# Kernel tuning notes

Measured on AMD Instinct MI355X. Metric: run time of the kernel, lower is better.

## Reference

```python
import jax, jax.numpy as jnp
import numpy as np
import math

H = 1024  # hidden_dim
NH = 16   # num_heads
HD = H // NH  # head_dim = 64
B, S, C = 2, 2048, 256  # batch, seq_len, cond_len
EPS = 1e-5


def layernorm(x, g, b):
    m = jnp.mean(x, axis=-1, keepdims=True)
    v = jnp.var(x, axis=-1, keepdims=True)
    return (x - m) * jax.lax.rsqrt(v + EPS) * g + b


def apply_rope(x, freqs):
    # x: [b, s, h, d], freqs broadcastable to [b, s, h, d//2]
    cos, sin = jnp.cos(freqs), jnp.sin(freqs)
    x1, x2 = jnp.split(x, 2, axis=-1)
    return jnp.concatenate([x1 * cos - x2 * sin, x2 * cos + x1 * sin], axis=-1)


def setup_inputs() -> dict:
    key = jax.random.key(0)
    ks = jax.random.split(key, 16)
    sc = 0.02
    x = jax.random.normal(ks[0], (B, S, H), jnp.float32)
    # rope freqs: positions * inv_freq over half head dim
    inv_freq = 1.0 / (10000.0 ** (jnp.arange(HD // 2, dtype=jnp.float32) / (HD // 2)))
    rope_freqs = (jnp.arange(S, dtype=jnp.float32)[:, None] * inv_freq[None, :]).reshape(S, 1, HD // 2)
    # causal additive mask [1,1,S,S]
    causal = jnp.tril(jnp.ones((S, S), dtype=bool))
    attention_mask = jnp.where(causal, 0.0, -1e9).astype(jnp.float32)[None, None]
    conditioning = jax.random.normal(ks[1], (B, C, H), jnp.float32)
    conditioning_mask = jnp.zeros((B, 1, 1, C), jnp.float32)
    params = dict(
        ln1_g=jnp.ones((H,)), ln1_b=jnp.zeros((H,)),
        ln2_g=jnp.ones((H,)), ln2_b=jnp.zeros((H,)),
        lnc_g=jnp.ones((H,)), lnc_b=jnp.zeros((H,)),
        w_qkv=jax.random.normal(ks[2], (H, 3 * H)) * sc,
        w_out=jax.random.normal(ks[3], (H, H)) * sc, b_out=jnp.zeros((H,)),
        w_cq=jax.random.normal(ks[4], (H, H)) * sc,
        w_ckv=jax.random.normal(ks[5], (H, 2 * H)) * sc,
        w_cout=jax.random.normal(ks[6], (H, H)) * sc, b_cout=jnp.zeros((H,)),
        w_ff1=jax.random.normal(ks[7], (H, 4 * H)) * sc, b_ff1=jnp.zeros((4 * H,)),
        w_ff2=jax.random.normal(ks[8], (4 * H, H)) * sc, b_ff2=jnp.zeros((H,)),
    )
    return dict(x=x, rope_freqs=rope_freqs, attention_mask=attention_mask,
                conditioning=conditioning, conditioning_mask=conditioning_mask, **params)


def reference(x, rope_freqs, attention_mask, conditioning, conditioning_mask,
              ln1_g, ln1_b, ln2_g, ln2_b, lnc_g, lnc_b,
              w_qkv, w_out, b_out, w_cq, w_ckv, w_cout, b_cout,
              w_ff1, b_ff1, w_ff2, b_ff2):
    scale = 1.0 / math.sqrt(HD)
    # --- causal self-attention ---
    residual = x
    h = layernorm(x, ln1_g, ln1_b)
    qkv = h @ w_qkv  # [b,s,3H]
    q, k, v = jnp.split(qkv, 3, axis=-1)
    q = q.reshape(B, S, NH, HD)
    k = k.reshape(B, S, NH, HD)
    v = v.reshape(B, S, NH, HD)
    q = apply_rope(q, rope_freqs)
    k = apply_rope(k, rope_freqs)
    scores = jnp.einsum('bqhd,bkhd->bhqk', q, k) * scale + attention_mask
    attn = jax.nn.softmax(scores, axis=-1)
    out = jnp.einsum('bhqk,bkhd->bqhd', attn, v).reshape(B, S, H)
    x = residual + out @ w_out + b_out
    # --- cross-attention ---
    residual = x
    h = layernorm(x, lnc_g, lnc_b)
    q = (h @ w_cq).reshape(B, S, NH, HD)
    kv = conditioning @ w_ckv
    k, v = jnp.split(kv, 2, axis=-1)
    k = k.reshape(B, C, NH, HD)
    v = v.reshape(B, C, NH, HD)
    scores = jnp.einsum('bqhd,bkhd->bhqk', q, k) * scale + conditioning_mask
    attn = jax.nn.softmax(scores, axis=-1)
    out = jnp.einsum('bhqk,bkhd->bqhd', attn, v).reshape(B, S, H)
    x = residual + out @ w_cout + b_cout
    # --- FFN ---
    residual = x
    h = layernorm(x, ln2_g, ln2_b)
    h = jax.nn.gelu(h @ w_ff1 + b_ff1, approximate=False)
    x = residual + h @ w_ff2 + b_ff2
    return x
```

## Files before the change

### kernel.cpp

```cpp
#include <hip/hip_runtime.h>

#define HDIM   1024
#define NHEADS 16
#define HEADD  64
#define BATCH  2
#define SEQ    2048
#define CLEN   256
#define NROWS  (BATCH*SEQ)
#define SCALE  0.125f

typedef __bf16 bf16x8 __attribute__((ext_vector_type(8)));
typedef float  f32x4  __attribute__((ext_vector_type(4)));

__device__ __forceinline__ unsigned short f2bf(float f) {
  union { float f; unsigned int u; } x; x.f = f;
  unsigned int r = x.u + 0x7fffu + ((x.u >> 16) & 1u);
  return (unsigned short)(r >> 16);
}
__device__ __forceinline__ float bf2f(unsigned short u) {
  union { unsigned int u; float f; } x; x.u = ((unsigned int)u) << 16;
  return x.f;
}

__device__ __forceinline__ void gl2lds16(const unsigned short* g, unsigned short* l) {
  __builtin_amdgcn_global_load_lds(
      (const __attribute__((address_space(1))) unsigned int*)g,
      (__attribute__((address_space(3))) unsigned int*)l, 16, 0, 0);
}

__global__ __launch_bounds__(256)
void cast_transpose64(const float* __restrict__ in, unsigned short* __restrict__ out,
                      int K, int N) {
  __shared__ float t[64][68];
  const int kb = blockIdx.y * 64, nb = blockIdx.x * 64;
  const int tid = threadIdx.x;
  const int r = tid >> 4, c = (tid & 15) * 4;
#pragma unroll
  for (int i = 0; i < 4; ++i) {
    float4 v = *(const float4*)(in + (size_t)(kb + r + i * 16) * N + nb + c);
    t[r + i * 16][c]     = v.x;
    t[r + i * 16][c + 1] = v.y;
    t[r + i * 16][c + 2] = v.z;
    t[r + i * 16][c + 3] = v.w;
  }
  __syncthreads();
  const int nr = tid >> 3, kc = (tid & 7) * 8;
#pragma unroll
  for (int i = 0; i < 2; ++i) {
    unsigned short us[8];
#pragma unroll
    for (int j = 0; j < 8; ++j) us[j] = f2bf(t[kc + j][nr + i * 32]);
    *(uint4*)(out + (size_t)(nb + nr + i * 32) * K + kb + kc) = *(uint4*)us;
  }
}

__global__ void cast_kernel8(const float* __restrict__ in, unsigned short* __restrict__ out, int n8) {
  int i = blockIdx.x * 256 + threadIdx.x;
  if (i < n8) {
    float4 a = ((const float4*)in)[2 * i], b = ((const float4*)in)[2 * i + 1];
    unsigned short us[8] = { f2bf(a.x), f2bf(a.y), f2bf(a.z), f2bf(a.w),
                             f2bf(b.x), f2bf(b.y), f2bf(b.z), f2bf(b.w) };
    ((uint4*)out)[i] = *(uint4*)us;
  }
}

__global__ __launch_bounds__(256)
void vtrans_kernel(const unsigned short* __restrict__ in, int str, int voff, int rows,
                   unsigned short* __restrict__ out) {
  __shared__ unsigned short t[64][72];
  const int h = blockIdx.y & (NHEADS - 1), b = blockIdx.y >> 4;
  const int s0 = blockIdx.x * 64;
  const int tid = threadIdx.x;
  const int r = tid >> 2, c = (tid & 3) * 16;
  const unsigned short* src = in + (size_t)(b * rows + s0 + r) * str + voff + h * 64 + c;
  *(uint4*)(&t[r][c])     = *(const uint4*)(src);
  *(uint4*)(&t[r][c + 8]) = *(const uint4*)(src + 8);
  __syncthreads();
  const int d = tid >> 2, sc = (tid & 3) * 16;
  unsigned short tmp[16];
#pragma unroll
  for (int i = 0; i < 16; ++i) tmp[i] = t[sc + i][d];
  unsigned short* dst = out + ((size_t)(b * NHEADS + h) * 64 + d) * rows + s0 + sc;
  *(uint4*)(dst)     = *(uint4*)(tmp);
  *(uint4*)(dst + 8) = *(uint4*)(tmp + 8);
}

__global__ __launch_bounds__(256)
void layernorm_kernel(const float* __restrict__ x, const float* __restrict__ g,
                      const float* __restrict__ b, unsigned short* __restrict__ out) {
  int row = blockIdx.x;
  const float4 v = ((const float4*)(x + (size_t)row * HDIM))[threadIdx.x];
  float s  = v.x + v.y + v.z + v.w;
  float sq = v.x*v.x + v.y*v.y + v.z*v.z + v.w*v.w;
  for (int o = 32; o; o >>= 1) { s += __shfl_xor(s, o); sq += __shfl_xor(sq, o); }
  __shared__ float rs[4], rq[4];
  int wave = threadIdx.x >> 6;
  if ((threadIdx.x & 63) == 0) { rs[wave] = s; rq[wave] = sq; }
  __syncthreads();
  s  = rs[0] + rs[1] + rs[2] + rs[3];
  sq = rq[0] + rq[1] + rq[2] + rq[3];
  float mean = s * (1.f/HDIM);
  float var  = sq * (1.f/HDIM) - mean*mean;
  float rstd = rsqrtf(var + 1e-5f);
  float4 gg = ((const float4*)g)[threadIdx.x];
  float4 bb = ((const float4*)b)[threadIdx.x];
  ushort4 o;
  o.x = f2bf((v.x - mean) * rstd * gg.x + bb.x);
  o.y = f2bf((v.y - mean) * rstd * gg.y + bb.y);
  o.z = f2bf((v.z - mean) * rstd * gg.z + bb.z);
  o.w = f2bf((v.w - mean) * rstd * gg.w + bb.w);
  ((ushort4*)(out + (size_t)row * HDIM))[threadIdx.x] = o;
}

template<int TBM, int TBN, bool BIAS, bool RES, bool GELU_, bool OUTBF>
__global__ __launch_bounds__(256)
void gemm_bt(const unsigned short* __restrict__ A, const unsigned short* __restrict__ Bt,
             const float* __restrict__ bias, const float* __restrict__ res,
             void* __restrict__ out, int M, int N, int K) {
  constexpr int MR = TBM / 32;
  constexpr int NR = TBN / 32;
  __shared__ unsigned short Al[2][TBM * 64];
  __shared__ unsigned short Bl[2][TBN * 64];
  const int tid  = threadIdx.x;
  const int wave = tid >> 6, lane = tid & 63;
  const int wr = wave >> 1, wc = wave & 1;
  const int nwg = gridDim.x * gridDim.y;
  int lin = blockIdx.y * gridDim.x + blockIdx.x;
  lin = (lin & 7) * (nwg >> 3) + (lin >> 3);
  const int m0 = (lin / gridDim.x) * TBM, n0 = (lin % gridDim.x) * TBN;
  const int lrow = lane & 15, hi = lane >> 4;
  const int rx = lrow & 7;

  f32x4 acc[MR][NR] = {};

  const int trow = tid >> 3, pslot = tid & 7;
  const int lcol = (pslot ^ (trow & 7)) * 8;
  const unsigned short* ga = A  + (size_t)(m0 + trow) * K + lcol;
  const unsigned short* gb = Bt + (size_t)(n0 + trow) * K + lcol;
  const int ldst = trow * 64 + pslot * 8;
  const int nt = K >> 6;

#pragma unroll
  for (int i = 0; i < MR; ++i)
    gl2lds16(ga + (size_t)i * 32 * K, Al[0] + ldst + i * 32 * 64);
#pragma unroll
  for (int i = 0; i < NR; ++i)
    gl2lds16(gb + (size_t)i * 32 * K, Bl[0] + ldst + i * 32 * 64);
  __syncthreads();

  int cur = 0;
  for (int t = 0; t < nt; ++t) {
    if (t + 1 < nt) {
      const int k1 = (t + 1) << 6;
#pragma unroll
      for (int i = 0; i < MR; ++i)
        gl2lds16(ga + (size_t)i * 32 * K + k1, Al[cur ^ 1] + ldst + i * 32 * 64);
#pragma unroll
      for (int i = 0; i < NR; ++i)
        gl2lds16(gb + (size_t)i * 32 * K + k1, Bl[cur ^ 1] + ldst + i * 32 * 64);
    }
#pragma unroll
    for (int kk = 0; kk < 2; ++kk) {
      const int cslot = ((kk << 2) | hi);
      const int coff  = (cslot ^ rx) * 8;
      bf16x8 af[MR], bfr[NR];
#pragma unroll
      for (int m = 0; m < MR; ++m)
        af[m] = *(const bf16x8*)(Al[cur] + (wr*(TBM/2) + m*16 + lrow) * 64 + coff);
#pragma unroll
      for (int n = 0; n < NR; ++n)
        bfr[n] = *(const bf16x8*)(Bl[cur] + (wc*(TBN/2) + n*16 + lrow) * 64 + coff);
#pragma unroll
      for (int m = 0; m < MR; ++m)
#pragma unroll
        for (int n = 0; n < NR; ++n)
          acc[m][n] = __builtin_amdgcn_mfma_f32_16x16x32_bf16(af[m], bfr[n], acc[m][n], 0, 0, 0);
    }
    __syncthreads();
    cur ^= 1;
  }

#pragma unroll
  for (int m = 0; m < MR; ++m)
#pragma unroll
    for (int n = 0; n < NR; ++n)
#pragma unroll
      for (int r = 0; r < 4; ++r) {
        int row = m0 + wr*(TBM/2) + m*16 + hi * 4 + r;
        int col = n0 + wc*(TBN/2) + n*16 + lrow;
        float v = acc[m][n][r];
        if (BIAS)  v += bias[col];
        if (GELU_) v = 0.5f * v * (1.0f + erff(v * 0.70710678118654752f));
        if (RES)   v += res[(size_t)row * N + col];
        if (OUTBF) ((unsigned short*)out)[(size_t)row * N + col] = f2bf(v);
        else       ((float*)out)[(size_t)row * N + col] = v;
      }
}

__global__ void rope_kernel(unsigned short* __restrict__ qkv, const float* __restrict__ freqs) {
  int idx = blockIdx.x * 256 + threadIdx.x;
  int d = idx & 31;
  int h = (idx >> 5) & 15;
  int row = idx >> 9;
  int s = row & (SEQ - 1);
  float f = freqs[s * 32 + d];
  float sn, cs;
  sincosf(f, &sn, &cs);
  size_t base = (size_t)row * 3072 + h * 64 + d;
  float x1 = bf2f(qkv[base]), x2 = bf2f(qkv[base + 32]);
  qkv[base]      = f2bf(x1 * cs - x2 * sn);
  qkv[base + 32] = f2bf(x2 * cs + x1 * sn);
  float y1 = bf2f(qkv[base + 1024]), y2 = bf2f(qkv[base + 1024 + 32]);
  qkv[base + 1024]      = f2bf(y1 * cs - y2 * sn);
  qkv[base + 1024 + 32] = f2bf(y2 * cs + y1 * sn);
}

#define QT 64
#define KT 64

__global__ __launch_bounds__(512)
void flash_attn_causal8(const unsigned short* __restrict__ qp, int qstr,
                        const unsigned short* __restrict__ kp, int kstr,
                        const unsigned short* __restrict__ vt,
                        unsigned short* __restrict__ outp) {
  __shared__ unsigned short Kl[2][KT][72];
  __shared__ unsigned short Vt[2][64][72];
  __shared__ unsigned short Pl[8][16][72];

  const int h = blockIdx.y & (NHEADS - 1), b = blockIdx.y >> 4;
  const int tid = threadIdx.x;
  const int wave = tid >> 6, lane = tid & 63;
  const int grp = wave >> 2, w4 = wave & 3;
  const int lo = lane & 15, hi = lane >> 4;
  const int NQB = SEQ / QT;
  float* mb = (float*)&Pl[0][0][0];

  const unsigned short* vbase = vt + (size_t)(b * NHEADS + h) * 64 * SEQ;

  for (int pass = 0; pass < 2; ++pass) {
    const int qblk = pass == 0 ? (int)blockIdx.x : NQB - 1 - (int)blockIdx.x;
    const int q0 = qblk * QT;
    const int qw = q0 + w4 * 16;

    bf16x8 qf[2];
    {
      const unsigned short* qb = qp + (size_t)(b * SEQ + qw + lo) * qstr + h * 64 + hi * 8;
      qf[0] = *(const bf16x8*)(qb);
      qf[1] = *(const bf16x8*)(qb + 32);
    }

    f32x4 o_acc[4] = {};
    float mrow[4], lrow[4];
#pragma unroll
    for (int r = 0; r < 4; ++r) { mrow[r] = -1e30f; lrow[r] = 0.f; }

    const int T = qblk + 1;
    const int iters = (T + 1) >> 1;
    for (int it = 0; it < iters; ++it) {
      const int t = 2 * it + grp;
      const bool act = t < T;
      const int j0 = t * KT;
      __syncthreads();
      if (act) {
        int tg = tid & 255;
        int r = tg >> 2, c = (tg & 3) * 16;
        const unsigned short* ksrc = kp + (size_t)(b * SEQ + j0 + r) * kstr + h * 64 + c;
        *(uint4*)(&Kl[grp][r][c])     = *(const uint4*)(ksrc);
        *(uint4*)(&Kl[grp][r][c + 8]) = *(const uint4*)(ksrc + 8);
        const unsigned short* vsrc = vbase + (size_t)r * SEQ + j0 + c;
        *(uint4*)(&Vt[grp][r][c])     = *(const uint4*)(vsrc);
        *(uint4*)(&Vt[grp][r][c + 8]) = *(const uint4*)(vsrc + 8);
      }
      __syncthreads();
      if (act) {
        f32x4 s[4] = {};
#pragma unroll
        for (int n = 0; n < 4; ++n) {
          bf16x8 b0 = *(const bf16x8*)(&Kl[grp][n * 16 + lo][hi * 8]);
          bf16x8 b1 = *(const bf16x8*)(&Kl[grp][n * 16 + lo][32 + hi * 8]);
          s[n] = __builtin_amdgcn_mfma_f32_16x16x32_bf16(qf[0], b0, s[n], 0, 0, 0);
          s[n] = __builtin_amdgcn_mfma_f32_16x16x32_bf16(qf[1], b1, s[n], 0, 0, 0);
        }
        if (t == T - 1) {
#pragma unroll
          for (int n = 0; n < 4; ++n)
#pragma unroll
            for (int r = 0; r < 4; ++r)
              if (j0 + n * 16 + lo > qw + hi * 4 + r) s[n][r] = -1e30f;
        }
        float pr[4][4];
#pragma unroll
        for (int r = 0; r < 4; ++r) {
          float mx = -1e30f;
#pragma unroll
          for (int n = 0; n < 4; ++n) {
            float v = s[n][r] * SCALE;
            s[n][r] = v;
            mx = fmaxf(mx, v);
          }
          mx = fmaxf(mx, __shfl_xor(mx, 1));
          mx = fmaxf(mx, __shfl_xor(mx, 2));
          mx = fmaxf(mx, __shfl_xor(mx, 4));
          mx = fmaxf(mx, __shfl_xor(mx, 8));
          const float mnew = fmaxf(mrow[r], mx);
          const float corr = __expf(mrow[r] - mnew);
          mrow[r] = mnew;
          float ls = 0.f;
#pragma unroll
          for (int n = 0; n < 4; ++n) {
            float p = __expf(s[n][r] - mnew);
            pr[n][r] = p;
            ls += p;
          }
          ls += __shfl_xor(ls, 1);
          ls += __shfl_xor(ls, 2);
          ls += __shfl_xor(ls, 4);
          ls += __shfl_xor(ls, 8);
          lrow[r] = lrow[r] * corr + ls;
#pragma unroll
          for (int n2 = 0; n2 < 4; ++n2) o_acc[n2][r] *= corr;
        }
#pragma unroll
        for (int n = 0; n < 4; ++n)
#pragma unroll
          for (int r = 0; r < 4; ++r)
            Pl[wave][hi * 4 + r][n * 16 + lo] = f2bf(pr[n][r]);

        bf16x8 pa0 = *(const bf16x8*)(&Pl[wave][lo][hi * 8]);
        bf16x8 pa1 = *(const bf16x8*)(&Pl[wave][lo][32 + hi * 8]);
#pragma unroll
        for (int n = 0; n < 4; ++n) {
          bf16x8 vb0 = *(const bf16x8*)(&Vt[grp][n * 16 + lo][hi * 8]);
          bf16x8 vb1 = *(const bf16x8*)(&Vt[grp][n * 16 + lo][32 + hi * 8]);
          o_acc[n] = __builtin_amdgcn_mfma_f32_16x16x32_bf16(pa0, vb0, o_acc[n], 0, 0, 0);
          o_acc[n] = __builtin_amdgcn_mfma_f32_16x16x32_bf16(pa1, vb1, o_acc[n], 0, 0, 0);
        }
      }
    }

    unsigned short* ob = outp + (size_t)(b * SEQ + qw) * HDIM + h * 64;
#pragma unroll
    for (int half = 0; half < 2; ++half) {
      __syncthreads();
      if (grp == 1) {
        float* dst = mb + (w4 * 64 + lane) * 13;
#pragma unroll
        for (int rr = 0; rr < 2; ++rr) {
          int r = half * 2 + rr;
          dst[rr * 6]     = mrow[r];
          dst[rr * 6 + 1] = lrow[r];
#pragma unroll
          for (int n = 0; n < 4; ++n) dst[rr * 6 + 2 + n] = o_acc[n][r];
        }
      }
      __syncthreads();
      if (grp == 0) {
        const float* s1 = mb + (w4 * 64 + lane) * 13;
#pragma unroll
        for (int rr = 0; rr < 2; ++rr) {
          int r = half * 2 + rr;
          float m1 = s1[rr * 6], l1 = s1[rr * 6 + 1];
          float M  = fmaxf(mrow[r], m1);
          float c0 = __expf(mrow[r] - M), c1 = __expf(m1 - M);
          float inv = 1.f / (lrow[r] * c0 + l1 * c1);
#pragma unroll
          for (int n = 0; n < 4; ++n) {
            float o = o_acc[n][r] * c0 + s1[rr * 6 + 2 + n] * c1;
            ob[(size_t)(hi * 4 + r) * HDIM + n * 16 + lo] = f2bf(o * inv);
          }
        }
      }
    }
    __syncthreads();
  }
}

__global__ __launch_bounds__(256)
void flash_attn_cross(const unsigned short* __restrict__ qp, int qstr,
                      const unsigned short* __restrict__ kp, int kstr,
                      const unsigned short* __restrict__ vt,
                      int kvrows, const float* __restrict__ mask,
                      unsigned short* __restrict__ outp) {
  __shared__ unsigned short Kl[KT][72];
  __shared__ unsigned short Vt[64][72];
  __shared__ unsigned short Pl[4][16][72];

  const int h = blockIdx.y & (NHEADS - 1), b = blockIdx.y >> 4;
  const int wave = threadIdx.x >> 6, lane = threadIdx.x & 63;
  const int lo = lane & 15, hi = lane >> 4;
  const int q0 = blockIdx.x * QT;
  const int qw = q0 + wave * 16;

  const unsigned short* vbase = vt + (size_t)(b * NHEADS + h) * 64 * kvrows;

  bf16x8 qf[2];
  {
    const unsigned short* qb = qp + (size_t)(b * SEQ + qw + lo) * qstr + h * 64 + hi * 8;
    qf[0] = *(const bf16x8*)(qb);
    qf[1] = *(const bf16x8*)(qb + 32);
  }

  f32x4 o_acc[4] = {};
  float mrow[4], lrow[4];
#pragma unroll
  for (int r = 0; r < 4; ++r) { mrow[r] = -1e30f; lrow[r] = 0.f; }

  const int ntiles = kvrows / KT;
  for (int t = 0; t < ntiles; ++t) {
    const int j0 = t * KT;
    __syncthreads();
    {
      int r = threadIdx.x >> 2, c = (threadIdx.x & 3) * 16;
      const unsigned short* ksrc = kp + (size_t)(b * kvrows + j0 + r) * kstr + h * 64 + c;
      *(uint4*)(&Kl[r][c])     = *(const uint4*)(ksrc);
      *(uint4*)(&Kl[r][c + 8]) = *(const uint4*)(ksrc + 8);
      const unsigned short* vsrc = vbase + (size_t)r * kvrows + j0 + c;
      *(uint4*)(&Vt[r][c])     = *(const uint4*)(vsrc);
      *(uint4*)(&Vt[r][c + 8]) = *(const uint4*)(vsrc + 8);
    }
    __syncthreads();

    f32x4 s[4] = {};
#pragma unroll
    for (int n = 0; n < 4; ++n) {
      bf16x8 b0 = *(const bf16x8*)(&Kl[n * 16 + lo][hi * 8]);
      bf16x8 b1 = *(const bf16x8*)(&Kl[n * 16 + lo][32 + hi * 8]);
      s[n] = __builtin_amdgcn_mfma_f32_16x16x32_bf16(qf[0], b0, s[n], 0, 0, 0);
      s[n] = __builtin_amdgcn_mfma_f32_16x16x32_bf16(qf[1], b1, s[n], 0, 0, 0);
    }

    float mk[4];
#pragma unroll
    for (int n = 0; n < 4; ++n) mk[n] = mask[b * kvrows + j0 + n * 16 + lo];

    float pr[4][4];
#pragma unroll
    for (int r = 0; r < 4; ++r) {
      float mx = -1e30f;
#pragma unroll
      for (int n = 0; n < 4; ++n) {
        float v = s[n][r] * SCALE + mk[n];
        s[n][r] = v;
        mx = fmaxf(mx, v);
      }
      mx = fmaxf(mx, __shfl_xor(mx, 1));
      mx = fmaxf(mx, __shfl_xor(mx, 2));
      mx = fmaxf(mx, __shfl_xor(mx, 4));
      mx = fmaxf(mx, __shfl_xor(mx, 8));
      const float mnew = fmaxf(mrow[r], mx);
      const float corr = __expf(mrow[r] - mnew);
      mrow[r] = mnew;
      float ls = 0.f;
#pragma unroll
      for (int n = 0; n < 4; ++n) {
        float p = __expf(s[n][r] - mnew);
        pr[n][r] = p;
        ls += p;
      }
      ls += __shfl_xor(ls, 1);
      ls += __shfl_xor(ls, 2);
      ls += __shfl_xor(ls, 4);
      ls += __shfl_xor(ls, 8);
      lrow[r] = lrow[r] * corr + ls;
#pragma unroll
      for (int n2 = 0; n2 < 4; ++n2) o_acc[n2][r] *= corr;
    }

#pragma unroll
    for (int n = 0; n < 4; ++n)
#pragma unroll
      for (int r = 0; r < 4; ++r)
        Pl[wave][hi * 4 + r][n * 16 + lo] = f2bf(pr[n][r]);

    bf16x8 pa0 = *(const bf16x8*)(&Pl[wave][lo][hi * 8]);
    bf16x8 pa1 = *(const bf16x8*)(&Pl[wave][lo][32 + hi * 8]);
#pragma unroll
    for (int n = 0; n < 4; ++n) {
      bf16x8 vb0 = *(const bf16x8*)(&Vt[n * 16 + lo][hi * 8]);
      bf16x8 vb1 = *(const bf16x8*)(&Vt[n * 16 + lo][32 + hi * 8]);
      o_acc[n] = __builtin_amdgcn_mfma_f32_16x16x32_bf16(pa0, vb0, o_acc[n], 0, 0, 0);
      o_acc[n] = __builtin_amdgcn_mfma_f32_16x16x32_bf16(pa1, vb1, o_acc[n], 0, 0, 0);
    }
  }

  unsigned short* ob = outp + (size_t)(b * SEQ + qw) * HDIM + h * 64;
#pragma unroll
  for (int r = 0; r < 4; ++r) {
    const float inv = 1.f / lrow[r];
#pragma unroll
    for (int n = 0; n < 4; ++n)
      ob[(size_t)(hi * 4 + r) * HDIM + n * 16 + lo] = f2bf(o_acc[n][r] * inv);
  }
}

extern "C" void kernel_launch(void* const* d_in, const int* in_sizes, int n_in,
                              void* d_out, int out_size, void* d_ws, size_t ws_size,
                              hipStream_t stream) {
  const float* x      = (const float*)d_in[0];
  const float* rfreq  = (const float*)d_in[1];
  const float* cond   = (const float*)d_in[3];
  const float* cmask  = (const float*)d_in[4];
  const float* ln1_g  = (const float*)d_in[5];
  const float* ln1_b  = (const float*)d_in[6];
  const float* ln2_g  = (const float*)d_in[7];
  const float* ln2_b  = (const float*)d_in[8];
  const float* lnc_g  = (const float*)d_in[9];
  const float* lnc_b  = (const float*)d_in[10];
  const float* w_qkv  = (const float*)d_in[11];
  const float* w_out  = (const float*)d_in[12];
  const float* b_out  = (const float*)d_in[13];
  const float* w_cq   = (const float*)d_in[14];
  const float* w_ckv  = (const float*)d_in[15];
  const float* w_cout = (const float*)d_in[16];
  const float* b_cout = (const float*)d_in[17];
  const float* w_ff1  = (const float*)d_in[18];
  const float* b_ff1  = (const float*)d_in[19];
  const float* w_ff2  = (const float*)d_in[20];
  const float* b_ff2  = (const float*)d_in[21];

  char* ws = (char*)d_ws;
  size_t off = 0;
  auto alloc = [&](size_t bytes) { size_t r = off; off += (bytes + 255) & ~(size_t)255; return r; };
  unsigned short* wt_qkv  = (unsigned short*)(ws + alloc((size_t)3072*1024*2));
  unsigned short* wt_out  = (unsigned short*)(ws + alloc((size_t)1024*1024*2));
  unsigned short* wt_cq   = (unsigned short*)(ws + alloc((size_t)1024*1024*2));
  unsigned short* wt_ckv  = (unsigned short*)(ws + alloc((size_t)2048*1024*2));
  unsigned short* wt_cout = (unsigned short*)(ws + alloc((size_t)1024*1024*2));
  unsigned short* wt_ff1  = (unsigned short*)(ws + alloc((size_t)4096*1024*2));
  unsigned short* wt_ff2  = (unsigned short*)(ws + alloc((size_t)1024*4096*2));
  unsigned short* condb   = (unsigned short*)(ws + alloc((size_t)512*1024*2));
  unsigned short* hbuf    = (unsigned short*)(ws + alloc((size_t)NROWS*1024*2));
  unsigned short* big     = (unsigned short*)(ws + alloc((size_t)NROWS*4096*2));
  unsigned short* attnb   = (unsigned short*)(ws + alloc((size_t)NROWS*1024*2));
  float*          x1      = (float*)(ws + alloc((size_t)NROWS*1024*4));
  unsigned short* kvc     = (unsigned short*)(ws + alloc((size_t)512*2048*2));
  unsigned short* vts     = (unsigned short*)(ws + alloc((size_t)BATCH*NHEADS*64*SEQ*2));
  unsigned short* vtc     = (unsigned short*)(ws + alloc((size_t)BATCH*NHEADS*64*CLEN*2));
  float*          outf    = (float*)d_out;

  cast_transpose64<<<dim3(48, 16), 256, 0, stream>>>(w_qkv,  wt_qkv,  1024, 3072);
  cast_transpose64<<<dim3(16, 16), 256, 0, stream>>>(w_out,  wt_out,  1024, 1024);
  cast_transpose64<<<dim3(16, 16), 256, 0, stream>>>(w_cq,   wt_cq,   1024, 1024);
  cast_transpose64<<<dim3(32, 16), 256, 0, stream>>>(w_ckv,  wt_ckv,  1024, 2048);
  cast_transpose64<<<dim3(16, 16), 256, 0, stream>>>(w_cout, wt_cout, 1024, 1024);
  cast_transpose64<<<dim3(64, 16), 256, 0, stream>>>(w_ff1,  wt_ff1,  1024, 4096);
  cast_transpose64<<<dim3(16, 64), 256, 0, stream>>>(w_ff2,  wt_ff2,  4096, 1024);
  cast_kernel8<<<(512*1024/8 + 255)/256, 256, 0, stream>>>(cond, condb, 512*1024/8);

  layernorm_kernel<<<NROWS, 256, 0, stream>>>(x, ln1_g, ln1_b, hbuf);
  gemm_bt<128,128,false,false,false,true><<<dim3(3072/128, NROWS/128), 256, 0, stream>>>(
      hbuf, wt_qkv, nullptr, nullptr, big, NROWS, 3072, 1024);
  rope_kernel<<<(NROWS*NHEADS*32)/256, 256, 0, stream>>>(big, rfreq);
  vtrans_kernel<<<dim3(SEQ/64, BATCH*NHEADS), 256, 0, stream>>>(big, 3072, 2048, SEQ, vts);
  flash_attn_causal8<<<dim3(SEQ/QT/2, BATCH*NHEADS), 512, 0, stream>>>(
      big, 3072, big + 1024, 3072, vts, attnb);
  gemm_bt<128,64,true,true,false,false><<<dim3(1024/64, NROWS/128), 256, 0, stream>>>(
      attnb, wt_out, b_out, x, x1, NROWS, 1024, 1024);

  layernorm_kernel<<<NROWS, 256, 0, stream>>>(x1, lnc_g, lnc_b, hbuf);
  gemm_bt<128,64,false,false,false,true><<<dim3(1024/64, NROWS/128), 256, 0, stream>>>(
      hbuf, wt_cq, nullptr, nullptr, big, NROWS, 1024, 1024);
  gemm_bt<64,64,false,false,false,true><<<dim3(2048/64, 512/64), 256, 0, stream>>>(
      condb, wt_ckv, nullptr, nullptr, kvc, 512, 2048, 1024);
  vtrans_kernel<<<dim3(CLEN/64, BATCH*NHEADS), 256, 0, stream>>>(kvc, 2048, 1024, CLEN, vtc);
  flash_attn_cross<<<dim3(SEQ/QT, BATCH*NHEADS), 256, 0, stream>>>(
      big, 1024, kvc, 2048, vtc, CLEN, cmask, attnb);
  gemm_bt<128,64,true,true,false,false><<<dim3(1024/64, NROWS/128), 256, 0, stream>>>(
      attnb, wt_cout, b_cout, x1, outf, NROWS, 1024, 1024);

  layernorm_kernel<<<NROWS, 256, 0, stream>>>(outf, ln2_g, ln2_b, hbuf);
  gemm_bt<128,128,true,false,true,true><<<dim3(4096/128, NROWS/128), 256, 0, stream>>>(
      hbuf, wt_ff1, b_ff1, nullptr, big, NROWS, 4096, 1024);
  gemm_bt<128,64,true,true,false,false><<<dim3(1024/64, NROWS/128), 256, 0, stream>>>(
      big, wt_ff2, b_ff2, outf, outf, NROWS, 1024, 4096);
}
```

Baseline: 370.3 us.

## Double-buffer flash attention K/V tiles via async global-to-LDS loads with swizzle

Replaces the 512-thread causal attention kernel, which split KV tiles across two wave groups and merged their partial results, with a 256-thread kernel. It double-buffers K/V tiles using direct global-to-LDS loads, prefetching the next tile while the current one is computed. LDS tiles now use an XOR-swizzled unpadded layout to avoid bank conflicts, and softmax uses exp2 with the log2e factor folded into the scale. The cross-attention kernel gets the same treatment. The trade-off is less intra-block parallelism per query block and one barrier per tile, in exchange for overlapped loads and no cross-group merge.

```diff
diff --git a/kernel.cpp b/kernel.cpp
--- a/kernel.cpp
+++ b/kernel.cpp
@@ -8,6 +8,7 @@
 #define CLEN   256
 #define NROWS  (BATCH*SEQ)
 #define SCALE  0.125f
+#define LOG2E  1.44269504088896f
 
 typedef __bf16 bf16x8 __attribute__((ext_vector_type(8)));
 typedef float  f32x4  __attribute__((ext_vector_type(4)));
@@ -215,32 +216,33 @@
   qkv[base + 1024 + 32] = f2bf(y2 * cs + y1 * sn);
 }
 
-#define QT 64
-#define KT 64
-
-__global__ __launch_bounds__(512)
-void flash_attn_causal8(const unsigned short* __restrict__ qp, int qstr,
+__global__ __launch_bounds__(256)
+void flash_attn_causal4(const unsigned short* __restrict__ qp, int qstr,
                         const unsigned short* __restrict__ kp, int kstr,
                         const unsigned short* __restrict__ vt,
                         unsigned short* __restrict__ outp) {
-  __shared__ unsigned short Kl[2][KT][72];
-  __shared__ unsigned short Vt[2][64][72];
-  __shared__ unsigned short Pl[8][16][72];
+  __shared__ unsigned short Kl[2][64 * 64];
+  __shared__ unsigned short Vl[2][64 * 64];
+  __shared__ unsigned short Pl[4][16][72];
 
   const int h = blockIdx.y & (NHEADS - 1), b = blockIdx.y >> 4;
   const int tid = threadIdx.x;
   const int wave = tid >> 6, lane = tid & 63;
-  const int grp = wave >> 2, w4 = wave & 3;
   const int lo = lane & 15, hi = lane >> 4;
-  const int NQB = SEQ / QT;
-  float* mb = (float*)&Pl[0][0][0];
+  const int NQB = SEQ / 64;
+  const float SC2 = SCALE * LOG2E;
 
   const unsigned short* vbase = vt + (size_t)(b * NHEADS + h) * 64 * SEQ;
+  const int trow = tid >> 3, pslot = tid & 7;
+  const int lcol = (pslot ^ (trow & 7)) * 8;
+  const int ldst = tid * 8;
+  const int x7 = lo & 7;
+  const int c0 = (hi ^ x7) * 8, c1 = ((hi + 4) ^ x7) * 8;
 
   for (int pass = 0; pass < 2; ++pass) {
     const int qblk = pass == 0 ? (int)blockIdx.x : NQB - 1 - (int)blockIdx.x;
-    const int q0 = qblk * QT;
-    const int qw = q0 + w4 * 16;
+    const int q0 = qblk * 64;
+    const int qw = q0 + wave * 16;
 
     bf16x8 qf[2];
     {
@@ -255,123 +257,105 @@
     for (int r = 0; r < 4; ++r) { mrow[r] = -1e30f; lrow[r] = 0.f; }
 
     const int T = qblk + 1;
-    const int iters = (T + 1) >> 1;
-    for (int it = 0; it < iters; ++it) {
-      const int t = 2 * it + grp;
-      const bool act = t < T;
-      const int j0 = t * KT;
+    {
+      const unsigned short* ks = kp + (size_t)(b * SEQ + trow) * kstr + h * 64 + lcol;
+      const unsigned short* vs = vbase + (size_t)trow * SEQ + lcol;
+      gl2lds16(ks, Kl[0] + ldst);
+      gl2lds16(ks + (size_t)32 * kstr, Kl[0] + ldst + 32 * 64);
+      gl2lds16(vs, Vl[0] + ldst);
+      gl2lds16(vs + (size_t)32 * SEQ, Vl[0] + ldst + 32 * 64);
+    }
+    __syncthreads();
+
+    int cur = 0;
+    for (int t = 0; t < T; ++t) {
+      if (t + 1 < T) {
+        const int j1 = (t + 1) * 64;
+        const unsigned short* ks = kp + (size_t)(b * SEQ + j1 + trow) * kstr + h * 64 + lcol;
+        const unsigned short* vs = vbase + (size_t)trow * SEQ + j1 + lcol;
+        gl2lds16(ks, Kl[cur ^ 1] + ldst);
+        gl2lds16(ks + (size_t)32 * kstr, Kl[cur ^ 1] + ldst + 32 * 64);
+        gl2lds16(vs, Vl[cur ^ 1] + ldst);
+        gl2lds16(vs + (size_t)32 * SEQ, Vl[cur ^ 1] + ldst + 32 * 64);
+      }
+      const unsigned short* Kc = Kl[cur];
+      const unsigned short* Vc = Vl[cur];
+      const int j0 = t * 64;
+
+      f32x4 s[4] = {};
+#pragma unroll
+      for (int n = 0; n < 4; ++n) {
+        bf16x8 b0 = *(const bf16x8*)(Kc + (n * 16 + lo) * 64 + c0);
+        bf16x8 b1 = *(const bf16x8*)(Kc + (n * 16 + lo) * 64 + c1);
+        s[n] = __builtin_amdgcn_mfma_f32_16x16x32_bf16(qf[0], b0, s[n], 0, 0, 0);
+        s[n] = __builtin_amdgcn_mfma_f32_16x16x32_bf16(qf[1], b1, s[n], 0, 0, 0);
+      }
+      if (t == T - 1) {
+#pragma unroll
+        for (int n = 0; n < 4; ++n)
+#pragma unroll
+          for (int r = 0; r < 4; ++r)
+            if (j0 + n * 16 + lo > qw + hi * 4 + r) s[n][r] = -1e30f;
+      }
+      float pr[4][4];
+#pragma unroll
+      for (int r = 0; r < 4; ++r) {
+        float mx = -1e30f;
+#pragma unroll
+        for (int n = 0; n < 4; ++n) {
+          float v = s[n][r] * SC2;
+          s[n][r] = v;
+          mx = fmaxf(mx, v);
+        }
+        mx = fmaxf(mx, __shfl_xor(mx, 1));
+        mx = fmaxf(mx, __shfl_xor(mx, 2));
+        mx = fmaxf(mx, __shfl_xor(mx, 4));
+        mx = fmaxf(mx, __shfl_xor(mx, 8));
+        const float mnew = fmaxf(mrow[r], mx);
+        const float corr = exp2f(mrow[r] - mnew);
+        mrow[r] = mnew;
+        float ls = 0.f;
+#pragma unroll
+        for (int n = 0; n < 4; ++n) {
+          float p = exp2f(s[n][r] - mnew);
+          pr[n][r] = p;
+          ls += p;
+        }
+        ls += __shfl_xor(ls, 1);
+        ls += __shfl_xor(ls, 2);
+        ls += __shfl_xor(ls, 4);
+        ls += __shfl_xor(ls, 8);
+        lrow[r] = lrow[r] * corr + ls;
+#pragma unroll
+        for (int n2 = 0; n2 < 4; ++n2) o_acc[n2][r] *= corr;
+      }
+#pragma unroll
+      for (int n = 0; n < 4; ++n)
+#pragma unroll
+        for (int r = 0; r < 4; ++r)
+          Pl[wave][hi * 4 + r][n * 16 + lo] = f2bf(pr[n][r]);
+
+      bf16x8 pa0 = *(const bf16x8*)(&Pl[wave][lo][hi * 8]);
+      bf16x8 pa1 = *(const bf16x8*)(&Pl[wave][lo][32 + hi * 8]);
+#pragma unroll
+      for (int n = 0; n < 4; ++n) {
+        bf16x8 vb0 = *(const bf16x8*)(Vc + (n * 16 + lo) * 64 + c0);
+        bf16x8 vb1 = *(const bf16x8*)(Vc + (n * 16 + lo) * 64 + c1);
+        o_acc[n] = __builtin_amdgcn_mfma_f32_16x16x32_bf16(pa0, vb0, o_acc[n], 0, 0, 0);
+        o_acc[n] = __builtin_amdgcn_mfma_f32_16x16x32_bf16(pa1, vb1, o_acc[n], 0, 0, 0);
+      }
       __syncthreads();
-      if (act) {
-        int tg = tid & 255;
-        int r = tg >> 2, c = (tg & 3) * 16;
-        const unsigned short* ksrc = kp + (size_t)(b * SEQ + j0 + r) * kstr + h * 64 + c;
-        *(uint4*)(&Kl[grp][r][c])     = *(const uint4*)(ksrc);
-        *(uint4*)(&Kl[grp][r][c + 8]) = *(const uint4*)(ksrc + 8);
-        const unsigned short* vsrc = vbase + (size_t)r * SEQ + j0 + c;
-        *(uint4*)(&Vt[grp][r][c])     = *(const uint4*)(vsrc);
-        *(uint4*)(&Vt[grp][r][c + 8]) = *(const uint4*)(vsrc + 8);
-      }
-      __syncthreads();
-      if (act) {
-        f32x4 s[4] = {};
-#pragma unroll
-        for (int n = 0; n < 4; ++n) {
-          bf16x8 b0 = *(const bf16x8*)(&Kl[grp][n * 16 + lo][hi * 8]);
-          bf16x8 b1 = *(const bf16x8*)(&Kl[grp][n * 16 + lo][32 + hi * 8]);
-          s[n] = __builtin_amdgcn_mfma_f32_16x16x32_bf16(qf[0], b0, s[n], 0, 0, 0);
-          s[n] = __builtin_amdgcn_mfma_f32_16x16x32_bf16(qf[1], b1, s[n], 0, 0, 0);
-        }
-        if (t == T - 1) {
-#pragma unroll
-          for (int n = 0; n < 4; ++n)
-#pragma unroll
-            for (int r = 0; r < 4; ++r)
-              if (j0 + n * 16 + lo > qw + hi * 4 + r) s[n][r] = -1e30f;
-        }
-        float pr[4][4];
-#pragma unroll
-        for (int r = 0; r < 4; ++r) {
-          float mx = -1e30f;
-#pragma unroll
-          for (int n = 0; n < 4; ++n) {
-            float v = s[n][r] * SCALE;
-            s[n][r] = v;
-            mx = fmaxf(mx, v);
-          }
-          mx = fmaxf(mx, __shfl_xor(mx, 1));
-          mx = fmaxf(mx, __shfl_xor(mx, 2));
-          mx = fmaxf(mx, __shfl_xor(mx, 4));
-          mx = fmaxf(mx, __shfl_xor(mx, 8));
-          const float mnew = fmaxf(mrow[r], mx);
-          const float corr = __expf(mrow[r] - mnew);
-          mrow[r] = mnew;
-          float ls = 0.f;
-#pragma unroll
-          for (int n = 0; n < 4; ++n) {
-            float p = __expf(s[n][r] - mnew);
-            pr[n][r] = p;
-            ls += p;
-          }
-          ls += __shfl_xor(ls, 1);
-          ls += __shfl_xor(ls, 2);
-          ls += __shfl_xor(ls, 4);
-          ls += __shfl_xor(ls, 8);
-          lrow[r] = lrow[r] * corr + ls;
-#pragma unroll
-          for (int n2 = 0; n2 < 4; ++n2) o_acc[n2][r] *= corr;
-        }
-#pragma unroll
-        for (int n = 0; n < 4; ++n)
-#pragma unroll
-          for (int r = 0; r < 4; ++r)
-            Pl[wave][hi * 4 + r][n * 16 + lo] = f2bf(pr[n][r]);
-
-        bf16x8 pa0 = *(const bf16x8*)(&Pl[wave][lo][hi * 8]);
-        bf16x8 pa1 = *(const bf16x8*)(&Pl[wave][lo][32 + hi * 8]);
-#pragma unroll
-        for (int n = 0; n < 4; ++n) {
-          bf16x8 vb0 = *(const bf16x8*)(&Vt[grp][n * 16 + lo][hi * 8]);
-          bf16x8 vb1 = *(const bf16x8*)(&Vt[grp][n * 16 + lo][32 + hi * 8]);
-          o_acc[n] = __builtin_amdgcn_mfma_f32_16x16x32_bf16(pa0, vb0, o_acc[n], 0, 0, 0);
-          o_acc[n] = __builtin_amdgcn_mfma_f32_16x16x32_bf16(pa1, vb1, o_acc[n], 0, 0, 0);
-        }
-      }
+      cur ^= 1;
     }
 
     unsigned short* ob = outp + (size_t)(b * SEQ + qw) * HDIM + h * 64;
 #pragma unroll
-    for (int half = 0; half < 2; ++half) {
-      __syncthreads();
-      if (grp == 1) {
-        float* dst = mb + (w4 * 64 + lane) * 13;
-#pragma unroll
-        for (int rr = 0; rr < 2; ++rr) {
-          int r = half * 2 + rr;
-          dst[rr * 6]     = mrow[r];
-          dst[rr * 6 + 1] = lrow[r];
-#pragma unroll
-          for (int n = 0; n < 4; ++n) dst[rr * 6 + 2 + n] = o_acc[n][r];
-        }
-      }
-      __syncthreads();
-      if (grp == 0) {
-        const float* s1 = mb + (w4 * 64 + lane) * 13;
-#pragma unroll
-        for (int rr = 0; rr < 2; ++rr) {
-          int r = half * 2 + rr;
-          float m1 = s1[rr * 6], l1 = s1[rr * 6 + 1];
-          float M  = fmaxf(mrow[r], m1);
-          float c0 = __expf(mrow[r] - M), c1 = __expf(m1 - M);
-          float inv = 1.f / (lrow[r] * c0 + l1 * c1);
-#pragma unroll
-          for (int n = 0; n < 4; ++n) {
-            float o = o_acc[n][r] * c0 + s1[rr * 6 + 2 + n] * c1;
-            ob[(size_t)(hi * 4 + r) * HDIM + n * 16 + lo] = f2bf(o * inv);
-          }
-        }
-      }
-    }
-    __syncthreads();
+    for (int r = 0; r < 4; ++r) {
+      const float inv = 1.f / lrow[r];
+#pragma unroll
+      for (int n = 0; n < 4; ++n)
+        ob[(size_t)(hi * 4 + r) * HDIM + n * 16 + lo] = f2bf(o_acc[n][r] * inv);
+    }
   }
 }
 
@@ -381,17 +365,24 @@
                       const unsigned short* __restrict__ vt,
                       int kvrows, const float* __restrict__ mask,
                       unsigned short* __restrict__ outp) {
-  __shared__ unsigned short Kl[KT][72];
-  __shared__ unsigned short Vt[64][72];
+  __shared__ unsigned short Kl[2][64 * 64];
+  __shared__ unsigned short Vl[2][64 * 64];
   __shared__ unsigned short Pl[4][16][72];
 
   const int h = blockIdx.y & (NHEADS - 1), b = blockIdx.y >> 4;
-  const int wave = threadIdx.x >> 6, lane = threadIdx.x & 63;
+  const int tid = threadIdx.x;
+  const int wave = tid >> 6, lane = tid & 63;
   const int lo = lane & 15, hi = lane >> 4;
-  const int q0 = blockIdx.x * QT;
-  const int qw = q0 + wave * 16;
+  const float SC2 = SCALE * LOG2E;
 
   const unsigned short* vbase = vt + (size_t)(b * NHEADS + h) * 64 * kvrows;
+  const int trow = tid >> 3, pslot = tid & 7;
+  const int lcol = (pslot ^ (trow & 7)) * 8;
+  const int ldst = tid * 8;
+  const int x7 = lo & 7;
+  const int c0 = (hi ^ x7) * 8, c1 = ((hi + 4) ^ x7) * 8;
+
+  const int qw = blockIdx.x * 64 + wave * 16;
 
   bf16x8 qf[2];
   {
@@ -405,33 +396,44 @@
 #pragma unroll
   for (int r = 0; r < 4; ++r) { mrow[r] = -1e30f; lrow[r] = 0.f; }
 
-  const int ntiles = kvrows / KT;
-  for (int t = 0; t < ntiles; ++t) {
-    const int j0 = t * KT;
-    __syncthreads();
-    {
-      int r = threadIdx.x >> 2, c = (threadIdx.x & 3) * 16;
-      const unsigned short* ksrc = kp + (size_t)(b * kvrows + j0 + r) * kstr + h * 64 + c;
-      *(uint4*)(&Kl[r][c])     = *(const uint4*)(ksrc);
-      *(uint4*)(&Kl[r][c + 8]) = *(const uint4*)(ksrc + 8);
-      const unsigned short* vsrc = vbase + (size_t)r * kvrows + j0 + c;
-      *(uint4*)(&Vt[r][c])     = *(const uint4*)(vsrc);
-      *(uint4*)(&Vt[r][c + 8]) = *(const uint4*)(vsrc + 8);
-    }
-    __syncthreads();
+  const int T = kvrows / 64;
+  {
+    const unsigned short* ks = kp + (size_t)(b * kvrows + trow) * kstr + h * 64 + lcol;
+    const unsigned short* vs = vbase + (size_t)trow * kvrows + lcol;
+    gl2lds16(ks, Kl[0] + ldst);
+    gl2lds16(ks + (size_t)32 * kstr, Kl[0] + ldst + 32 * 64);
+    gl2lds16(vs, Vl[0] + ldst);
+    gl2lds16(vs + (size_t)32 * kvrows, Vl[0] + ldst + 32 * 64);
+  }
+  __syncthreads();
+
+  int cur = 0;
+  for (int t = 0; t < T; ++t) {
+    if (t + 1 < T) {
+      const int j1 = (t + 1) * 64;
+      const unsigned short* ks = kp + (size_t)(b * kvrows + j1 + trow) * kstr + h * 64 + lcol;
+      const unsigned short* vs = vbase + (size_t)trow * kvrows + j1 + lcol;
+      gl2lds16(ks, Kl[cur ^ 1] + ldst);
+      gl2lds16(ks + (size_t)32 * kstr, Kl[cur ^ 1] + ldst + 32 * 64);
+      gl2lds16(vs, Vl[cur ^ 1] + ldst);
+      gl2lds16(vs + (size_t)32 * kvrows, Vl[cur ^ 1] + ldst + 32 * 64);
+    }
+    const unsigned short* Kc = Kl[cur];
+    const unsigned short* Vc = Vl[cur];
+    const int j0 = t * 64;
 
     f32x4 s[4] = {};
 #pragma unroll
     for (int n = 0; n < 4; ++n) {
-      bf16x8 b0 = *(const bf16x8*)(&Kl[n * 16 + lo][hi * 8]);
-      bf16x8 b1 = *(const bf16x8*)(&Kl[n * 16 + lo][32 + hi * 8]);
+      bf16x8 b0 = *(const bf16x8*)(Kc + (n * 16 + lo) * 64 + c0);
+      bf16x8 b1 = *(const bf16x8*)(Kc + (n * 16 + lo) * 64 + c1);
       s[n] = __builtin_amdgcn_mfma_f32_16x16x32_bf16(qf[0], b0, s[n], 0, 0, 0);
       s[n] = __builtin_amdgcn_mfma_f32_16x16x32_bf16(qf[1], b1, s[n], 0, 0, 0);
     }
 
-    float mk[4];
-#pragma unroll
-    for (int n = 0; n < 4; ++n) mk[n] = mask[b * kvrows + j0 + n * 16 + lo];
+    float mk2[4];
+#pragma unroll
+    for (int n = 0; n < 4; ++n) mk2[n] = mask[b * kvrows + j0 + n * 16 + lo] * LOG2E;
 
     float pr[4][4];
 #pragma unroll
@@ -439,7 +441,7 @@
       float mx = -1e30f;
 #pragma unroll
       for (int n = 0; n < 4; ++n) {
-        float v = s[n][r] * SCALE + mk[n];
+        float v = s[n][r] * SC2 + mk2[n];
         s[n][r] = v;
         mx = fmaxf(mx, v);
       }
@@ -448,12 +450,12 @@
       mx = fmaxf(mx, __shfl_xor(mx, 4));
       mx = fmaxf(mx, __shfl_xor(mx, 8));
       const float mnew = fmaxf(mrow[r], mx);
-      const float corr = __expf(mrow[r] - mnew);
+      const float corr = exp2f(mrow[r] - mnew);
       mrow[r] = mnew;
       float ls = 0.f;
 #pragma unroll
       for (int n = 0; n < 4; ++n) {
-        float p = __expf(s[n][r] - mnew);
+        float p = exp2f(s[n][r] - mnew);
         pr[n][r] = p;
         ls += p;
       }
@@ -476,11 +478,13 @@
     bf16x8 pa1 = *(const bf16x8*)(&Pl[wave][lo][32 + hi * 8]);
 #pragma unroll
     for (int n = 0; n < 4; ++n) {
-      bf16x8 vb0 = *(const bf16x8*)(&Vt[n * 16 + lo][hi * 8]);
-      bf16x8 vb1 = *(const bf16x8*)(&Vt[n * 16 + lo][32 + hi * 8]);
+      bf16x8 vb0 = *(const bf16x8*)(Vc + (n * 16 + lo) * 64 + c0);
+      bf16x8 vb1 = *(const bf16x8*)(Vc + (n * 16 + lo) * 64 + c1);
       o_acc[n] = __builtin_amdgcn_mfma_f32_16x16x32_bf16(pa0, vb0, o_acc[n], 0, 0, 0);
       o_acc[n] = __builtin_amdgcn_mfma_f32_16x16x32_bf16(pa1, vb1, o_acc[n], 0, 0, 0);
     }
+    __syncthreads();
+    cur ^= 1;
   }
 
   unsigned short* ob = outp + (size_t)(b * SEQ + qw) * HDIM + h * 64;
@@ -552,7 +556,7 @@
       hbuf, wt_qkv, nullptr, nullptr, big, NROWS, 3072, 1024);
   rope_kernel<<<(NROWS*NHEADS*32)/256, 256, 0, stream>>>(big, rfreq);
   vtrans_kernel<<<dim3(SEQ/64, BATCH*NHEADS), 256, 0, stream>>>(big, 3072, 2048, SEQ, vts);
-  flash_attn_causal8<<<dim3(SEQ/QT/2, BATCH*NHEADS), 512, 0, stream>>>(
+  flash_attn_causal4<<<dim3(SEQ/64/2, BATCH*NHEADS), 256, 0, stream>>>(
       big, 3072, big + 1024, 3072, vts, attnb);
   gemm_bt<128,64,true,true,false,false><<<dim3(1024/64, NROWS/128), 256, 0, stream>>>(
       attnb, wt_out, b_out, x, x1, NROWS, 1024, 1024);
@@ -563,7 +567,7 @@
   gemm_bt<64,64,false,false,false,true><<<dim3(2048/64, 512/64), 256, 0, stream>>>(
       condb, wt_ckv, nullptr, nullptr, kvc, 512, 2048, 1024);
   vtrans_kernel<<<dim3(CLEN/64, BATCH*NHEADS), 256, 0, stream>>>(kvc, 2048, 1024, CLEN, vtc);
-  flash_attn_cross<<<dim3(SEQ/QT, BATCH*NHEADS), 256, 0, stream>>>(
+  flash_attn_cross<<<dim3(SEQ/64, BATCH*NHEADS), 256, 0, stream>>>(
       big, 1024, kvc, 2048, vtc, CLEN, cmask, attnb);
   gemm_bt<128,64,true,true,false,false><<<dim3(1024/64, NROWS/128), 256, 0, stream>>>(
       attnb, wt_cout, b_cout, x1, outf, NROWS, 1024, 1024);
```

Measured after the change: 388.9 us. +5.0%, slower.
